# Performance work log

Measured on AMD Instinct MI355X. Metric: run time of the kernel, lower is better.

The kernel has to match this reference:

```python
import math
import jax, jax.numpy as jnp
import numpy as np

VERY_NEGATIVE_NUMBER = -1e29
HEADS = 16
UNITS = 1024
INPUT_DIM = 1024
B, LQ, LK = 2, 2048, 2048


def setup_inputs() -> dict:
    key = jax.random.key(0)
    ks = jax.random.split(key, 8)
    s = 1.0 / math.sqrt(INPUT_DIM)
    return {
        "query": jax.random.normal(ks[0], (B, LQ, INPUT_DIM), jnp.float32),
        "key": jax.random.normal(ks[1], (B, LK, INPUT_DIM), jnp.float32),
        "value": jax.random.normal(ks[2], (B, LK, INPUT_DIM), jnp.float32),
        "key_mask": jax.random.randint(ks[3], (B, LK), 0, 2, jnp.int32),
        "Wq": jax.random.normal(ks[4], (INPUT_DIM, UNITS), jnp.float32) * s,
        "bq": jnp.zeros((UNITS,), jnp.float32),
        "Wk": jax.random.normal(ks[5], (INPUT_DIM, UNITS), jnp.float32) * s,
        "bk": jnp.zeros((UNITS,), jnp.float32),
        "Wv": jax.random.normal(ks[6], (INPUT_DIM, UNITS), jnp.float32) * s,
        "bv": jnp.zeros((UNITS,), jnp.float32),
    }


def reference(query, key, value, key_mask, Wq, bq, Wk, bk, Wv, bv):
    b, lq, lk = query.shape[0], query.shape[1], key.shape[1]
    h = HEADS
    d = UNITS // h  # head dim
    # projections -> [B, L, H, D]
    wq = (query @ Wq + bq).reshape(b, lq, h, d)
    wk = (key @ Wk + bk).reshape(b, lk, h, d)
    wv = (value @ Wv + bv).reshape(b, lk, h, d)
    scale = 1.0 / math.sqrt(float(UNITS) / h)
    # scores laid out [H, B, Q, K] as in the torch code
    scores = jnp.einsum("bqhd,bkhd->hbqk", wq, wk) * scale
    # additive key mask, broadcast [1, B, 1, K]
    km = key_mask.astype(scores.dtype)
    scores = scores + (1.0 - km)[None, :, None, :] * VERY_NEGATIVE_NUMBER
    sim = jax.nn.softmax(scores, axis=-1)
    out = jnp.einsum("hbqk,bkhd->bqhd", sim, wv).reshape(b, lq, UNITS)
    return out
```

## Files before the change

kernel.cpp:

```cpp
#include <hip/hip_runtime.h>
#include <cstdint>
#include <cstddef>

typedef __attribute__((ext_vector_type(4))) float f32x4;
typedef __attribute__((ext_vector_type(8))) short bf16x8;
typedef __attribute__((ext_vector_type(4))) unsigned int u32x4;

#define QSCALE 0.18033688011112042f
#define NSHIFT 17.3123404906676f

static __device__ __forceinline__ unsigned short f2bf(float f) {
    return (unsigned short)((__builtin_bit_cast(unsigned int, f) + 0x8000u) >> 16);
}
static __device__ __forceinline__ unsigned int pk2(float a, float b) {
    unsigned int ua = __builtin_bit_cast(unsigned int, a) + 0x8000u;
    unsigned int ub = __builtin_bit_cast(unsigned int, b) + 0x8000u;
    return (ua >> 16) | (ub & 0xffff0000u);
}
static __device__ __forceinline__ unsigned int pack2h(float a, float b) {
    unsigned int ua = __builtin_bit_cast(unsigned int, a) + 0x8000u;
    unsigned int ub = __builtin_bit_cast(unsigned int, b) + 0x8000u;
    return __builtin_amdgcn_perm(ub, ua, 0x07060302);
}
static __device__ __forceinline__ void glds16(const unsigned short* g, unsigned short* l) {
    __builtin_amdgcn_global_load_lds((const __attribute__((address_space(1))) void*)g,
                                     (__attribute__((address_space(3))) void*)l, 16, 0, 0);
}

__global__ __launch_bounds__(256) void prep(
    const float* __restrict__ Wq, const float* __restrict__ Wk, const float* __restrict__ Wv,
    const float* __restrict__ Xq, const float* __restrict__ Xk, const float* __restrict__ Xv,
    unsigned short* __restrict__ Wt, unsigned short* __restrict__ Xb)
{
    const int z = blockIdx.y;
    if (blockIdx.x < 1024) {
        __shared__ float tile[32][33];
        const float* W = (z == 0) ? Wq : (z == 1) ? Wk : Wv;
        unsigned short* dst = Wt + (size_t)z * 1048576;
        int n0 = (blockIdx.x & 31) * 32, k0 = (blockIdx.x >> 5) * 32;
        int tx = threadIdx.x & 31, ty = threadIdx.x >> 5;
#pragma unroll
        for (int i = 0; i < 32; i += 8)
            tile[ty + i][tx] = W[(size_t)(k0 + ty + i) * 1024 + n0 + tx];
        __syncthreads();
#pragma unroll
        for (int i = 0; i < 32; i += 8)
            dst[(size_t)(n0 + ty + i) * 1024 + k0 + tx] = f2bf(tile[tx][ty + i]);
    } else {
        const float* X = (z == 0) ? Xq : (z == 1) ? Xk : Xv;
        unsigned short* dst = Xb + (size_t)z * 4194304;
        size_t base = (size_t)(blockIdx.x - 1024) * 2048 + threadIdx.x * 8;
        float4 a = *(const float4*)&X[base];
        float4 c = *(const float4*)&X[base + 4];
        *(int4*)&dst[base] = make_int4(pk2(a.x, a.y), pk2(a.z, a.w),
                                       pk2(c.x, c.y), pk2(c.z, c.w));
    }
}

__global__ __launch_bounds__(256, 3) void proj_g(
    const unsigned short* __restrict__ Xb, const unsigned short* __restrict__ Wt,
    const float* __restrict__ bq, const float* __restrict__ bk, const float* __restrict__ bv,
    const int* __restrict__ km, unsigned short* __restrict__ packs)
{
    const int mode = blockIdx.z;
    const unsigned short* X = Xb + (size_t)mode * 4194304;
    const unsigned short* W = Wt + (size_t)mode * 1048576;
    const float* bias = (mode == 0) ? bq : (mode == 1) ? bk : bv;
    unsigned short* outp = packs + (size_t)mode * 4194304;

    __shared__ alignas(16) unsigned short As[128 * 64];
    __shared__ alignas(16) unsigned short Bs[128 * 64];

    const int tid = threadIdx.x, wid = tid >> 6, lane = tid & 63;
    const int lrow = lane & 15, g = lane >> 4;
    const int m0 = blockIdx.x * 128, n0 = blockIdx.y * 128;
    const int wr = (wid >> 1) * 64, wc = (wid & 1) * 64;
    const int srow = tid >> 3;
    const int scol = ((tid & 7) ^ (srow & 7)) * 8;
    const int sdst = srow * 64 + (tid & 7) * 8;

    f32x4 acc[4][4] = {};

    for (int k0 = 0; k0 < 1024; k0 += 64) {
        __syncthreads();
#pragma unroll
        for (int p = 0; p < 4; ++p)
            glds16(&X[(size_t)(m0 + p * 32 + srow) * 1024 + k0 + scol], &As[p * 2048 + sdst]);
#pragma unroll
        for (int p = 0; p < 4; ++p)
            glds16(&W[(size_t)(n0 + p * 32 + srow) * 1024 + k0 + scol], &Bs[p * 2048 + sdst]);
        asm volatile("s_waitcnt vmcnt(0)" ::: "memory");
        __syncthreads();

#pragma unroll
        for (int kk = 0; kk < 2; ++kk) {
            bf16x8 af[4], bfr[4];
#pragma unroll
            for (int i = 0; i < 4; ++i)
                af[i] = *(const bf16x8*)&As[(wr + i * 16 + lrow) * 64 + (((kk * 4 + g) ^ (lrow & 7)) * 8)];
#pragma unroll
            for (int j = 0; j < 4; ++j)
                bfr[j] = *(const bf16x8*)&Bs[(wc + j * 16 + lrow) * 64 + (((kk * 4 + g) ^ (lrow & 7)) * 8)];
#pragma unroll
            for (int i = 0; i < 4; ++i)
#pragma unroll
                for (int j = 0; j < 4; ++j)
                    acc[i][j] = __builtin_amdgcn_mfma_f32_16x16x32_bf16(af[i], bfr[j], acc[i][j], 0, 0, 0);
        }
    }

#pragma unroll
    for (int j = 0; j < 4; ++j) {
        int n = n0 + wc + j * 16 + lrow;
        float bv_ = bias[n];
        int h = n >> 6, d = n & 63;
#pragma unroll
        for (int i = 0; i < 4; ++i) {
#pragma unroll
            for (int r = 0; r < 4; ++r) {
                int m = m0 + wr + i * 16 + g * 4 + r;
                float val = acc[i][j][r] + bv_;
                if (mode == 0) val *= QSCALE;
                int b = m >> 11, l = m & 2047;
                size_t idx;
                if (mode == 2) {
                    val *= (float)km[m];
                    idx = (((size_t)((b << 4) + h) << 6) + d) * 2048 + l;
                } else {
                    idx = (((size_t)((b << 4) + h) << 11) + l) * 64 + d;
                }
                outp[idx] = f2bf(val);
            }
        }
    }
}

__global__ __launch_bounds__(256) void transpose_w3(
    const float* __restrict__ Wq, const float* __restrict__ Wk,
    const float* __restrict__ Wv, unsigned short* __restrict__ Wt)
{
    __shared__ float tile[32][33];
    const float* W = (blockIdx.z == 0) ? Wq : (blockIdx.z == 1) ? Wk : Wv;
    unsigned short* dst = Wt + (size_t)blockIdx.z * 1048576;
    int tx = threadIdx.x & 31, ty = threadIdx.x >> 5;
    int n0 = blockIdx.x * 32, k0 = blockIdx.y * 32;
#pragma unroll
    for (int i = 0; i < 32; i += 8)
        tile[ty + i][tx] = W[(size_t)(k0 + ty + i) * 1024 + n0 + tx];
    __syncthreads();
#pragma unroll
    for (int i = 0; i < 32; i += 8)
        dst[(size_t)(n0 + ty + i) * 1024 + k0 + tx] = f2bf(tile[tx][ty + i]);
}

__global__ __launch_bounds__(256, 3) void proj_fb(
    const float* __restrict__ Xq, const float* __restrict__ Xk, const float* __restrict__ Xv,
    const unsigned short* __restrict__ Wt,
    const float* __restrict__ bq, const float* __restrict__ bk, const float* __restrict__ bv,
    const int* __restrict__ km, unsigned short* __restrict__ packs)
{
    const int mode = blockIdx.z;
    const float* X = (mode == 0) ? Xq : (mode == 1) ? Xk : Xv;
    const unsigned short* W = Wt + (size_t)mode * 1048576;
    const float* bias = (mode == 0) ? bq : (mode == 1) ? bk : bv;
    unsigned short* outp = packs + (size_t)mode * 4194304;

    __shared__ alignas(16) unsigned short As[128 * 64];
    __shared__ alignas(16) unsigned short Bs[128 * 64];

    const int tid = threadIdx.x, wid = tid >> 6, lane = tid & 63;
    const int lrow = lane & 15, g = lane >> 4;
    const int m0 = blockIdx.x * 128, n0 = blockIdx.y * 128;
    const int wr = (wid >> 1) * 64, wc = (wid & 1) * 64;
    const int srow = tid >> 3;
    const int scol = ((tid & 7) ^ (srow & 7)) * 8;
    const int sdst = srow * 64 + (tid & 7) * 8;
    const int ar = tid >> 2;
    const int acb = (tid & 3) * 2;

    f32x4 acc[4][4] = {};

    for (int k0 = 0; k0 < 1024; k0 += 64) {
        __syncthreads();
#pragma unroll
        for (int p = 0; p < 4; ++p)
            glds16(&W[(size_t)(n0 + p * 32 + srow) * 1024 + k0 + scol], &Bs[p * 2048 + sdst]);
#pragma unroll
        for (int p = 0; p < 2; ++p) {
            int r = p * 64 + ar;
#pragma unroll
            for (int bl = 0; bl < 2; ++bl) {
                int cb = acb + bl;
                const float* src = &X[(size_t)(m0 + r) * 1024 + k0 + cb * 8];
                float4 v0 = *(const float4*)src;
                float4 v1 = *(const float4*)(src + 4);
                *(int4*)&As[r * 64 + ((cb ^ (r & 7)) * 8)] =
                    make_int4(pk2(v0.x, v0.y), pk2(v0.z, v0.w),
                              pk2(v1.x, v1.y), pk2(v1.z, v1.w));
            }
        }
        asm volatile("s_waitcnt vmcnt(0)" ::: "memory");
        __syncthreads();

#pragma unroll
        for (int kk = 0; kk < 2; ++kk) {
            bf16x8 af[4], bfr[4];
#pragma unroll
            for (int i = 0; i < 4; ++i)
                af[i] = *(const bf16x8*)&As[(wr + i * 16 + lrow) * 64 + (((kk * 4 + g) ^ (lrow & 7)) * 8)];
#pragma unroll
            for (int j = 0; j < 4; ++j)
                bfr[j] = *(const bf16x8*)&Bs[(wc + j * 16 + lrow) * 64 + (((kk * 4 + g) ^ (lrow & 7)) * 8)];
#pragma unroll
            for (int i = 0; i < 4; ++i)
#pragma unroll
                for (int j = 0; j < 4; ++j)
                    acc[i][j] = __builtin_amdgcn_mfma_f32_16x16x32_bf16(af[i], bfr[j], acc[i][j], 0, 0, 0);
        }
    }

#pragma unroll
    for (int j = 0; j < 4; ++j) {
        int n = n0 + wc + j * 16 + lrow;
        float bv_ = bias[n];
        int h = n >> 6, d = n & 63;
#pragma unroll
        for (int i = 0; i < 4; ++i) {
#pragma unroll
            for (int r = 0; r < 4; ++r) {
                int m = m0 + wr + i * 16 + g * 4 + r;
                float val = acc[i][j][r] + bv_;
                if (mode == 0) val *= QSCALE;
                int b = m >> 11, l = m & 2047;
                size_t idx;
                if (mode == 2) {
                    val *= (float)km[m];
                    idx = (((size_t)((b << 4) + h) << 6) + d) * 2048 + l;
                } else {
                    idx = (((size_t)((b << 4) + h) << 11) + l) * 64 + d;
                }
                outp[idx] = f2bf(val);
            }
        }
    }
}

__global__ __launch_bounds__(256, 2) void attn(
    const unsigned short* __restrict__ Qp, const unsigned short* __restrict__ Kp,
    const unsigned short* __restrict__ Vtp, const int* __restrict__ km_g,
    float* __restrict__ out)
{
    __shared__ alignas(16) unsigned short Ks[2][128 * 64];
    __shared__ alignas(16) unsigned short Vs[2][64 * 128];
    __shared__ alignas(16) unsigned short Ms[2048];

    const int tid = threadIdx.x, wid = tid >> 6, lane = tid & 63;
    const int lrow = lane & 15, g = lane >> 4;
    const int bh = blockIdx.y, b = bh >> 4, h = bh & 15;
    const int q0 = blockIdx.x * 128;
    const unsigned short* Q = Qp + (size_t)bh * 131072;
    const unsigned short* K = Kp + (size_t)bh * 131072;
    const unsigned short* V = Vtp + (size_t)bh * 131072;

    const int sr = lane >> 3;
    const int sc = ((lane & 7) ^ sr) * 8;
    const int sw = (lane & 7) * 8;

    {
        const int* km = km_g + b * 2048;
        int4 a = *(const int4*)&km[tid * 8];
        int4 c = *(const int4*)&km[tid * 8 + 4];
        unsigned int w0 = (a.x ? 0x3F80u : 0u) | ((a.y ? 0x3F80u : 0u) << 16);
        unsigned int w1 = (a.z ? 0x3F80u : 0u) | ((a.w ? 0x3F80u : 0u) << 16);
        unsigned int w2 = (c.x ? 0x3F80u : 0u) | ((c.y ? 0x3F80u : 0u) << 16);
        unsigned int w3 = (c.z ? 0x3F80u : 0u) | ((c.w ? 0x3F80u : 0u) << 16);
        *(int4*)&Ms[tid * 8] = make_int4(w0, w1, w2, w3);
    }

    bf16x8 qf[2][2];
#pragma unroll
    for (int qs = 0; qs < 2; ++qs) {
        const unsigned short* qrow = Q + (size_t)(q0 + wid * 32 + qs * 16 + lrow) * 64;
        qf[qs][0] = *(const bf16x8*)(qrow + g * 8);
        qf[qs][1] = *(const bf16x8*)(qrow + 32 + g * 8);
    }

    const int kr0 = wid * 16 + sr, kr1 = kr0 + 8;
    const int pk0 = ((kr0 >> 4) & 1) * 32 + ((kr0 >> 2) & 3) * 8 + ((kr0 >> 5) & 1) * 4 + (kr0 & 3);
    const int pk1 = ((kr1 >> 4) & 1) * 32 + ((kr1 >> 2) & 3) * 8 + ((kr1 >> 5) & 1) * 4 + (kr1 & 3);

    auto STAGE = [&](int buf, int kt) {
#pragma unroll
        for (int c = 0; c < 2; ++c) {
            glds16(&K[(size_t)(kt + c * 64 + pk0) * 64 + sc], &Ks[buf][(c * 64 + kr0) * 64 + sw]);
            glds16(&K[(size_t)(kt + c * 64 + pk1) * 64 + sc], &Ks[buf][(c * 64 + kr1) * 64 + sw]);
        }
#pragma unroll
        for (int i = 0; i < 4; ++i) {
            const int dbase = wid * 16 + i * 4;
            const int d = dbase + (lane >> 4);
            const int vc = (lane >> 3) & 1;
            const int b8 = lane & 7;
            glds16(&V[(size_t)d * 2048 + kt + vc * 64 + ((b8 ^ (d & 7)) * 8)],
                   &Vs[buf][dbase * 128 + lane * 8]);
        }
    };

    f32x4 accO[2][4] = {};
    f32x4 accL[2] = {};
    const f32x4 sinit = {-NSHIFT, -NSHIFT, -NSHIFT, -NSHIFT};

    STAGE(0, 0);
    for (int t = 0; t < 16; ++t) {
        const int cur = t & 1, kt = t * 128;
        asm volatile("s_waitcnt vmcnt(0)" ::: "memory");
        __syncthreads();
        if (t < 15) STAGE(cur ^ 1, kt + 128);

#pragma unroll
        for (int half = 0; half < 2; ++half) {
            const int kb = half * 64;

            f32x4 accS[2][4];
#pragma unroll
            for (int s = 0; s < 4; ++s) {
                const int krow = kb + s * 16 + lrow;
                bf16x8 kf0 = *(const bf16x8*)&Ks[cur][krow * 64 + ((g ^ (lrow & 7)) * 8)];
                bf16x8 kf1 = *(const bf16x8*)&Ks[cur][krow * 64 + (((4 + g) ^ (lrow & 7)) * 8)];
#pragma unroll
                for (int qs = 0; qs < 2; ++qs) {
                    accS[qs][s] = __builtin_amdgcn_mfma_f32_16x16x32_bf16(kf0, qf[qs][0], sinit, 0, 0, 0);
                    accS[qs][s] = __builtin_amdgcn_mfma_f32_16x16x32_bf16(kf1, qf[qs][1], accS[qs][s], 0, 0, 0);
                }
            }

            bf16x8 pf[2][2];
#pragma unroll
            for (int qs = 0; qs < 2; ++qs) {
                float e0[4], e1[4], e2[4], e3[4];
#pragma unroll
                for (int r = 0; r < 4; ++r) {
                    e0[r] = exp2f(accS[qs][0][r]);
                    e1[r] = exp2f(accS[qs][1][r]);
                    e2[r] = exp2f(accS[qs][2][r]);
                    e3[r] = exp2f(accS[qs][3][r]);
                }
                u32x4 t0 = {pack2h(e0[0], e0[1]), pack2h(e0[2], e0[3]),
                            pack2h(e2[0], e2[1]), pack2h(e2[2], e2[3])};
                u32x4 t1 = {pack2h(e1[0], e1[1]), pack2h(e1[2], e1[3]),
                            pack2h(e3[0], e3[1]), pack2h(e3[2], e3[3])};
                pf[qs][0] = __builtin_bit_cast(bf16x8, t0);
                pf[qs][1] = __builtin_bit_cast(bf16x8, t1);
            }

            bf16x8 mf0 = *(const bf16x8*)&Ms[kt + kb + g * 8];
            bf16x8 mf1 = *(const bf16x8*)&Ms[kt + kb + 32 + g * 8];
#pragma unroll
            for (int qs = 0; qs < 2; ++qs) {
                accL[qs] = __builtin_amdgcn_mfma_f32_16x16x32_bf16(pf[qs][0], mf0, accL[qs], 0, 0, 0);
                accL[qs] = __builtin_amdgcn_mfma_f32_16x16x32_bf16(pf[qs][1], mf1, accL[qs], 0, 0, 0);
            }

#pragma unroll
            for (int j = 0; j < 4; ++j) {
                const int vrow = (j * 16 + lrow) * 128 + kb;
                bf16x8 vf0 = *(const bf16x8*)&Vs[cur][vrow + ((g ^ (lrow & 7)) * 8)];
                bf16x8 vf1 = *(const bf16x8*)&Vs[cur][vrow + (((4 + g) ^ (lrow & 7)) * 8)];
#pragma unroll
                for (int qs = 0; qs < 2; ++qs) {
                    accO[qs][j] = __builtin_amdgcn_mfma_f32_16x16x32_bf16(pf[qs][0], vf0, accO[qs][j], 0, 0, 0);
                    accO[qs][j] = __builtin_amdgcn_mfma_f32_16x16x32_bf16(pf[qs][1], vf1, accO[qs][j], 0, 0, 0);
                }
            }
        }
    }

#pragma unroll
    for (int qs = 0; qs < 2; ++qs)
#pragma unroll
        for (int j = 0; j < 4; ++j)
#pragma unroll
            for (int r = 0; r < 4; ++r) {
                int qq = q0 + wid * 32 + qs * 16 + g * 4 + r;
                out[((size_t)(b * 2048 + qq)) * 1024 + h * 64 + j * 16 + lrow] =
                    accO[qs][j][r] / accL[qs][r];
            }
}

extern "C" void kernel_launch(void* const* d_in, const int* in_sizes, int n_in,
                              void* d_out, int out_size, void* d_ws, size_t ws_size,
                              hipStream_t stream) {
    const float* query    = (const float*)d_in[0];
    const float* key      = (const float*)d_in[1];
    const float* value    = (const float*)d_in[2];
    const int*   key_mask = (const int*)d_in[3];
    const float* Wq = (const float*)d_in[4];
    const float* bq = (const float*)d_in[5];
    const float* Wk = (const float*)d_in[6];
    const float* bk = (const float*)d_in[7];
    const float* Wv = (const float*)d_in[8];
    const float* bv = (const float*)d_in[9];
    float* out = (float*)d_out;

    char* ws = (char*)d_ws;
    unsigned short* Wt = (unsigned short*)ws;
    unsigned short* Pk = (unsigned short*)(ws + 6291456);
    unsigned short* Xb = (unsigned short*)(ws + 31457280);

    if (ws_size >= 56623104ull) {
        prep<<<dim3(3072, 3), 256, 0, stream>>>(Wq, Wk, Wv, query, key, value, Wt, Xb);
        proj_g<<<dim3(32, 8, 3), 256, 0, stream>>>(Xb, Wt, bq, bk, bv, key_mask, Pk);
    } else {
        transpose_w3<<<dim3(32, 32, 3), 256, 0, stream>>>(Wq, Wk, Wv, Wt);
        proj_fb<<<dim3(32, 8, 3), 256, 0, stream>>>(query, key, value, Wt, bq, bk, bv, key_mask, Pk);
    }
    attn<<<dim3(16, 32), 256, 0, stream>>>(Pk, Pk + 4194304, Pk + 8388608, key_mask, out);
}
```

Measured before the change: 126.8 us.

## Shrink attention blocks to two waves and 64-key tiles, add setprio and fast exp2

The attention kernel now runs 128-thread blocks covering 64 queries each, over 1024 blocks instead of 512, and streams K/V in 64-key tiles across 32 iterations. The staging loads are rewritten to match the smaller tiles. The MFMA phases are wrapped in s_setprio so waves doing matrix work get issue priority. exp2f is replaced with the raw hardware exp2 builtin. The aim is more blocks in flight and less LDS per block for better occupancy, at the cost of twice as many barriers and loop iterations.

```diff
diff --git a/kernel.cpp b/kernel.cpp
--- a/kernel.cpp
+++ b/kernel.cpp
@@ -22,6 +22,11 @@
     unsigned int ub = __builtin_bit_cast(unsigned int, b) + 0x8000u;
     return __builtin_amdgcn_perm(ub, ua, 0x07060302);
 }
+#if __has_builtin(__builtin_amdgcn_exp2f)
+static __device__ __forceinline__ float fexp2(float x) { return __builtin_amdgcn_exp2f(x); }
+#else
+static __device__ __forceinline__ float fexp2(float x) { return exp2f(x); }
+#endif
 static __device__ __forceinline__ void glds16(const unsigned short* g, unsigned short* l) {
     __builtin_amdgcn_global_load_lds((const __attribute__((address_space(1))) void*)g,
                                      (__attribute__((address_space(3))) void*)l, 16, 0, 0);
@@ -245,36 +250,38 @@
     }
 }
 
-__global__ __launch_bounds__(256, 2) void attn(
+__global__ __launch_bounds__(128, 2) void attn(
     const unsigned short* __restrict__ Qp, const unsigned short* __restrict__ Kp,
     const unsigned short* __restrict__ Vtp, const int* __restrict__ km_g,
     float* __restrict__ out)
 {
-    __shared__ alignas(16) unsigned short Ks[2][128 * 64];
-    __shared__ alignas(16) unsigned short Vs[2][64 * 128];
+    __shared__ alignas(16) unsigned short Ks[2][64 * 64];
+    __shared__ alignas(16) unsigned short Vs[2][64 * 64];
     __shared__ alignas(16) unsigned short Ms[2048];
 
     const int tid = threadIdx.x, wid = tid >> 6, lane = tid & 63;
     const int lrow = lane & 15, g = lane >> 4;
     const int bh = blockIdx.y, b = bh >> 4, h = bh & 15;
-    const int q0 = blockIdx.x * 128;
+    const int q0 = blockIdx.x * 64;
     const unsigned short* Q = Qp + (size_t)bh * 131072;
     const unsigned short* K = Kp + (size_t)bh * 131072;
     const unsigned short* V = Vtp + (size_t)bh * 131072;
 
     const int sr = lane >> 3;
-    const int sc = ((lane & 7) ^ sr) * 8;
-    const int sw = (lane & 7) * 8;
+    const int b8 = lane & 7;
+    const int sc = (b8 ^ sr) * 8;
 
     {
         const int* km = km_g + b * 2048;
-        int4 a = *(const int4*)&km[tid * 8];
-        int4 c = *(const int4*)&km[tid * 8 + 4];
-        unsigned int w0 = (a.x ? 0x3F80u : 0u) | ((a.y ? 0x3F80u : 0u) << 16);
-        unsigned int w1 = (a.z ? 0x3F80u : 0u) | ((a.w ? 0x3F80u : 0u) << 16);
-        unsigned int w2 = (c.x ? 0x3F80u : 0u) | ((c.y ? 0x3F80u : 0u) << 16);
-        unsigned int w3 = (c.z ? 0x3F80u : 0u) | ((c.w ? 0x3F80u : 0u) << 16);
-        *(int4*)&Ms[tid * 8] = make_int4(w0, w1, w2, w3);
+        unsigned int w[8];
+#pragma unroll
+        for (int p = 0; p < 4; ++p) {
+            int4 a = *(const int4*)&km[tid * 16 + p * 4];
+            w[p * 2]     = (a.x ? 0x3F80u : 0u) | ((a.y ? 0x3F80u : 0u) << 16);
+            w[p * 2 + 1] = (a.z ? 0x3F80u : 0u) | ((a.w ? 0x3F80u : 0u) << 16);
+        }
+        *(int4*)&Ms[tid * 16]     = make_int4(w[0], w[1], w[2], w[3]);
+        *(int4*)&Ms[tid * 16 + 8] = make_int4(w[4], w[5], w[6], w[7]);
     }
 
     bf16x8 qf[2][2];
@@ -285,24 +292,17 @@
         qf[qs][1] = *(const bf16x8*)(qrow + 32 + g * 8);
     }
 
-    const int kr0 = wid * 16 + sr, kr1 = kr0 + 8;
-    const int pk0 = ((kr0 >> 4) & 1) * 32 + ((kr0 >> 2) & 3) * 8 + ((kr0 >> 5) & 1) * 4 + (kr0 & 3);
-    const int pk1 = ((kr1 >> 4) & 1) * 32 + ((kr1 >> 2) & 3) * 8 + ((kr1 >> 5) & 1) * 4 + (kr1 & 3);
-
     auto STAGE = [&](int buf, int kt) {
 #pragma unroll
-        for (int c = 0; c < 2; ++c) {
-            glds16(&K[(size_t)(kt + c * 64 + pk0) * 64 + sc], &Ks[buf][(c * 64 + kr0) * 64 + sw]);
-            glds16(&K[(size_t)(kt + c * 64 + pk1) * 64 + sc], &Ks[buf][(c * 64 + kr1) * 64 + sw]);
-        }
-#pragma unroll
         for (int i = 0; i < 4; ++i) {
-            const int dbase = wid * 16 + i * 4;
-            const int d = dbase + (lane >> 4);
-            const int vc = (lane >> 3) & 1;
-            const int b8 = lane & 7;
-            glds16(&V[(size_t)d * 2048 + kt + vc * 64 + ((b8 ^ (d & 7)) * 8)],
-                   &Vs[buf][dbase * 128 + lane * 8]);
+            const int vr = wid * 32 + i * 8 + sr;
+            const int pk = ((vr >> 4) & 1) * 32 + ((vr >> 2) & 3) * 8 + ((vr >> 5) & 1) * 4 + (vr & 3);
+            glds16(&K[(size_t)(kt + pk) * 64 + sc], &Ks[buf][vr * 64 + b8 * 8]);
+        }
+#pragma unroll
+        for (int i = 0; i < 4; ++i) {
+            const int d = wid * 32 + i * 8 + sr;
+            glds16(&V[(size_t)d * 2048 + kt + sc], &Vs[buf][d * 64 + b8 * 8]);
         }
     };
 
@@ -311,68 +311,67 @@
     const f32x4 sinit = {-NSHIFT, -NSHIFT, -NSHIFT, -NSHIFT};
 
     STAGE(0, 0);
-    for (int t = 0; t < 16; ++t) {
-        const int cur = t & 1, kt = t * 128;
+    for (int t = 0; t < 32; ++t) {
+        const int cur = t & 1, kt = t * 64;
         asm volatile("s_waitcnt vmcnt(0)" ::: "memory");
         __syncthreads();
-        if (t < 15) STAGE(cur ^ 1, kt + 128);
-
-#pragma unroll
-        for (int half = 0; half < 2; ++half) {
-            const int kb = half * 64;
-
-            f32x4 accS[2][4];
-#pragma unroll
-            for (int s = 0; s < 4; ++s) {
-                const int krow = kb + s * 16 + lrow;
-                bf16x8 kf0 = *(const bf16x8*)&Ks[cur][krow * 64 + ((g ^ (lrow & 7)) * 8)];
-                bf16x8 kf1 = *(const bf16x8*)&Ks[cur][krow * 64 + (((4 + g) ^ (lrow & 7)) * 8)];
-#pragma unroll
-                for (int qs = 0; qs < 2; ++qs) {
-                    accS[qs][s] = __builtin_amdgcn_mfma_f32_16x16x32_bf16(kf0, qf[qs][0], sinit, 0, 0, 0);
-                    accS[qs][s] = __builtin_amdgcn_mfma_f32_16x16x32_bf16(kf1, qf[qs][1], accS[qs][s], 0, 0, 0);
-                }
-            }
-
-            bf16x8 pf[2][2];
+        if (t < 31) STAGE(cur ^ 1, kt + 64);
+
+        bf16x8 mf0 = *(const bf16x8*)&Ms[kt + g * 8];
+        bf16x8 mf1 = *(const bf16x8*)&Ms[kt + 32 + g * 8];
+
+        f32x4 accS[2][4];
+        __builtin_amdgcn_s_setprio(1);
+#pragma unroll
+        for (int s = 0; s < 4; ++s) {
+            const int krow = s * 16 + lrow;
+            bf16x8 kf0 = *(const bf16x8*)&Ks[cur][krow * 64 + ((g ^ (lrow & 7)) * 8)];
+            bf16x8 kf1 = *(const bf16x8*)&Ks[cur][krow * 64 + (((4 + g) ^ (lrow & 7)) * 8)];
 #pragma unroll
             for (int qs = 0; qs < 2; ++qs) {
-                float e0[4], e1[4], e2[4], e3[4];
-#pragma unroll
-                for (int r = 0; r < 4; ++r) {
-                    e0[r] = exp2f(accS[qs][0][r]);
-                    e1[r] = exp2f(accS[qs][1][r]);
-                    e2[r] = exp2f(accS[qs][2][r]);
-                    e3[r] = exp2f(accS[qs][3][r]);
-                }
-                u32x4 t0 = {pack2h(e0[0], e0[1]), pack2h(e0[2], e0[3]),
-                            pack2h(e2[0], e2[1]), pack2h(e2[2], e2[3])};
-                u32x4 t1 = {pack2h(e1[0], e1[1]), pack2h(e1[2], e1[3]),
-                            pack2h(e3[0], e3[1]), pack2h(e3[2], e3[3])};
-                pf[qs][0] = __builtin_bit_cast(bf16x8, t0);
-                pf[qs][1] = __builtin_bit_cast(bf16x8, t1);
-            }
-
-            bf16x8 mf0 = *(const bf16x8*)&Ms[kt + kb + g * 8];
-            bf16x8 mf1 = *(const bf16x8*)&Ms[kt + kb + 32 + g * 8];
+                accS[qs][s] = __builtin_amdgcn_mfma_f32_16x16x32_bf16(kf0, qf[qs][0], sinit, 0, 0, 0);
+                accS[qs][s] = __builtin_amdgcn_mfma_f32_16x16x32_bf16(kf1, qf[qs][1], accS[qs][s], 0, 0, 0);
+            }
+        }
+        __builtin_amdgcn_s_setprio(0);
+
+        bf16x8 pf[2][2];
+#pragma unroll
+        for (int qs = 0; qs < 2; ++qs) {
+            float e0[4], e1[4], e2[4], e3[4];
+#pragma unroll
+            for (int r = 0; r < 4; ++r) {
+                e0[r] = fexp2(accS[qs][0][r]);
+                e1[r] = fexp2(accS[qs][1][r]);
+                e2[r] = fexp2(accS[qs][2][r]);
+                e3[r] = fexp2(accS[qs][3][r]);
+            }
+            u32x4 t0 = {pack2h(e0[0], e0[1]), pack2h(e0[2], e0[3]),
+                        pack2h(e2[0], e2[1]), pack2h(e2[2], e2[3])};
+            u32x4 t1 = {pack2h(e1[0], e1[1]), pack2h(e1[2], e1[3]),
+                        pack2h(e3[0], e3[1]), pack2h(e3[2], e3[3])};
+            pf[qs][0] = __builtin_bit_cast(bf16x8, t0);
+            pf[qs][1] = __builtin_bit_cast(bf16x8, t1);
+        }
+
+        __builtin_amdgcn_s_setprio(1);
+#pragma unroll
+        for (int qs = 0; qs < 2; ++qs) {
+            accL[qs] = __builtin_amdgcn_mfma_f32_16x16x32_bf16(pf[qs][0], mf0, accL[qs], 0, 0, 0);
+            accL[qs] = __builtin_amdgcn_mfma_f32_16x16x32_bf16(pf[qs][1], mf1, accL[qs], 0, 0, 0);
+        }
+#pragma unroll
+        for (int j = 0; j < 4; ++j) {
+            const int vrow = (j * 16 + lrow) * 64;
+            bf16x8 vf0 = *(const bf16x8*)&Vs[cur][vrow + ((g ^ (lrow & 7)) * 8)];
+            bf16x8 vf1 = *(const bf16x8*)&Vs[cur][vrow + (((4 + g) ^ (lrow & 7)) * 8)];
 #pragma unroll
             for (int qs = 0; qs < 2; ++qs) {
-                accL[qs] = __builtin_amdgcn_mfma_f32_16x16x32_bf16(pf[qs][0], mf0, accL[qs], 0, 0, 0);
-                accL[qs] = __builtin_amdgcn_mfma_f32_16x16x32_bf16(pf[qs][1], mf1, accL[qs], 0, 0, 0);
-            }
-
-#pragma unroll
-            for (int j = 0; j < 4; ++j) {
-                const int vrow = (j * 16 + lrow) * 128 + kb;
-                bf16x8 vf0 = *(const bf16x8*)&Vs[cur][vrow + ((g ^ (lrow & 7)) * 8)];
-                bf16x8 vf1 = *(const bf16x8*)&Vs[cur][vrow + (((4 + g) ^ (lrow & 7)) * 8)];
-#pragma unroll
-                for (int qs = 0; qs < 2; ++qs) {
-                    accO[qs][j] = __builtin_amdgcn_mfma_f32_16x16x32_bf16(pf[qs][0], vf0, accO[qs][j], 0, 0, 0);
-                    accO[qs][j] = __builtin_amdgcn_mfma_f32_16x16x32_bf16(pf[qs][1], vf1, accO[qs][j], 0, 0, 0);
-                }
-            }
-        }
+                accO[qs][j] = __builtin_amdgcn_mfma_f32_16x16x32_bf16(pf[qs][0], vf0, accO[qs][j], 0, 0, 0);
+                accO[qs][j] = __builtin_amdgcn_mfma_f32_16x16x32_bf16(pf[qs][1], vf1, accO[qs][j], 0, 0, 0);
+            }
+        }
+        __builtin_amdgcn_s_setprio(0);
     }
 
 #pragma unroll
@@ -414,5 +413,5 @@
         transpose_w3<<<dim3(32, 32, 3), 256, 0, stream>>>(Wq, Wk, Wv, Wt);
         proj_fb<<<dim3(32, 8, 3), 256, 0, stream>>>(query, key, value, Wt, bq, bk, bv, key_mask, Pk);
     }
-    attn<<<dim3(16, 32), 256, 0, stream>>>(Pk, Pk + 4194304, Pk + 8388608, key_mask, out);
-}
+    attn<<<dim3(32, 32), 128, 0, stream>>>(Pk, Pk + 4194304, Pk + 8388608, key_mask, out);
+}
```

Result: faster. 113.6 us (-10.4%).
